# Optimization experiments

Hardware: AMD Instinct MI355X
Metric: run time of the kernel (lower is better)

## Reference

```python
import jax, jax.numpy as jnp
import numpy as np

PAD = 1  # deform_conv2d called with stride=1, padding=1, dilation=1 in forward


def _bilinear_gather(x, py, px):
    """Bilinear sample x [B,C,H,W] at float coords py,px [B,K,Ho,Wo].
    Out-of-bounds corners contribute zero (torchvision deform_conv2d semantics).
    Returns [B,C,K,Ho,Wo]."""
    B, C, H, W = x.shape
    y0 = jnp.floor(py)
    x0 = jnp.floor(px)
    y1, x1 = y0 + 1.0, x0 + 1.0
    wy1 = py - y0
    wy0 = 1.0 - wy1
    wx1 = px - x0
    wx0 = 1.0 - wx1
    x_flat = x.reshape(B, C, H * W)

    def corner(yi, xi, w):
        m = ((yi >= 0) & (yi < H) & (xi >= 0) & (xi < W)).astype(x.dtype)
        yc = jnp.clip(yi, 0, H - 1).astype(jnp.int32)
        xc = jnp.clip(xi, 0, W - 1).astype(jnp.int32)
        lin = (yc * W + xc).reshape(B, -1)  # [B, K*Ho*Wo]
        vals = jax.vmap(lambda xf, idx: jnp.take(xf, idx, axis=1))(x_flat, lin)
        vals = vals.reshape(B, C, *yi.shape[1:])  # [B,C,K,Ho,Wo]
        return vals * (w * m)[:, None]

    return (corner(y0, x0, wy0 * wx0) + corner(y0, x1, wy0 * wx1)
            + corner(y1, x0, wy1 * wx0) + corner(y1, x1, wy1 * wx1))


def reference(x, w_off, b_off, weight):
    B, C, H, W = x.shape
    O, Ci, kh, kw = weight.shape
    K = kh * kw
    # offset conv: Conv2d(C -> 2*k*k, kernel 3, stride 1, pad 1, groups=1)
    offset = jax.lax.conv_general_dilated(
        x, w_off, window_strides=(1, 1), padding=[(PAD, PAD), (PAD, PAD)],
        dimension_numbers=('NCHW', 'OIHW', 'NCHW')) + b_off[None, :, None, None]
    off = offset.reshape(B, K, 2, H, W)  # channel layout: (tap, [dy, dx])

    ky = jnp.repeat(jnp.arange(kh, dtype=x.dtype), kw)  # [K] kernel row index
    kx = jnp.tile(jnp.arange(kw, dtype=x.dtype), kh)    # [K] kernel col index
    ys = jnp.arange(H, dtype=x.dtype)[None, None, :, None]  # [1,1,H,1]
    xs = jnp.arange(W, dtype=x.dtype)[None, None, None, :]  # [1,1,1,W]
    py = ys + (ky - PAD)[None, :, None, None] + off[:, :, 0]  # [B,K,H,W]
    px = xs + (kx - PAD)[None, :, None, None] + off[:, :, 1]

    sampled = _bilinear_gather(x, py, px)  # [B,C,K,H,W]
    out = jnp.einsum('bckhw,ock->bohw', sampled, weight.reshape(O, Ci, K))
    return out


def setup_inputs() -> dict:
    key = jax.random.key(0)
    k1, k2, k3 = jax.random.split(key, 3)
    x = jax.random.normal(k1, (4, 64, 128, 128), dtype=jnp.float32)
    # small offset-conv weights -> modest learned offsets (realistic DCN behavior)
    w_off = jax.random.normal(k2, (18, 64, 3, 3), dtype=jnp.float32) * 0.01
    b_off = jnp.zeros((18,), dtype=jnp.float32)
    weight = jax.random.normal(k3, (64, 64, 3, 3), dtype=jnp.float32)
    return {'x': x, 'w_off': w_off, 'b_off': b_off, 'weight': weight}
```

## Files before the change

### kernel.cpp

```cpp
#include <hip/hip_runtime.h>
#include <math.h>

typedef _Float16 f16;
typedef _Float16 f16x8 __attribute__((ext_vector_type(8)));
typedef float f32x4 __attribute__((ext_vector_type(4)));

namespace {
constexpr int Bn = 4;
constexpr int Cn = 64;
constexpr int On = 64;
constexpr int Hn = 128;
constexpr int Wn = 128;
constexpr int Kn = 9;
constexpr int HWn = Hn * Wn;
constexpr int CKn = Cn * Kn;
constexpr int NPIX = Bn * HWn;
constexpr int SR = 72;
}

__global__ __launch_bounds__(256) void prep_weights(
    const float* __restrict__ w_off, const float* __restrict__ weight,
    f16* __restrict__ wofb, f16* __restrict__ wtb) {
  int t = blockIdx.x * 256 + threadIdx.x;
  if (t < Kn * On * Cn) {
    int c = t & 63, o = (t >> 6) & 63, k = t >> 12;
    wtb[t] = (f16)weight[((o << 6) + c) * 9 + k];
  }
  if (t < Kn * 32 * Cn) {
    int c = t & 63, o = (t >> 6) & 31, k = t >> 11;
    float v = (o < 18) ? w_off[((o << 6) + c) * 9 + k] : 0.f;
    wofb[t] = (f16)v;
  }
}

__global__ __launch_bounds__(256) void transpose_x(
    const float* __restrict__ x, f16* __restrict__ xt) {
  const int l = threadIdx.x & 63;
  const int cw = threadIdx.x >> 6;
  const int pixbase = blockIdx.x * 64;
  const int b = pixbase >> 14;
  const int hw = (pixbase & (HWn - 1)) + l;

  f16x8 v0, v1;
#pragma unroll
  for (int i = 0; i < 8; ++i) {
    v0[i] = (f16)x[((size_t)(b * Cn + cw * 16 + i)) * HWn + hw];
    v1[i] = (f16)x[((size_t)(b * Cn + cw * 16 + 8 + i)) * HWn + hw];
  }
  f16* dst = xt + ((size_t)(b * HWn + hw)) * 64 + cw * 16;
  *(f16x8*)dst = v0;
  *(f16x8*)(dst + 8) = v1;
}

__global__ __launch_bounds__(256) void offset_mfma(
    const f16* __restrict__ xt, const f16* __restrict__ wofb,
    const float* __restrict__ b_off, float* __restrict__ offset) {
  __shared__ __align__(16) f16 Sb[2][64 * SR];
  __shared__ __align__(16) f16 Wb[2][32 * SR];

  const int t = threadIdx.x;
  const int pixbase = blockIdx.x * 64;
  const int b = pixbase >> 14;
  const int y = (pixbase & (HWn - 1)) >> 7;
  const int xx0 = pixbase & (Wn - 1);
  const f16* xb = xt + ((size_t)b * HWn) * 64;

  const int px_s = t >> 2, cq = t & 3;
  const int lane = t & 63, wv = t >> 6;
  const int l15 = lane & 15, q = lane >> 4;
  const int m = wv & 1;
  const int nb = (wv >> 1) * 2;

  auto stage = [&](int k, int buf) {
    const int dy = k / 3 - 1, dx = k % 3 - 1;
    const int ys = y + dy, xs = xx0 + px_s + dx;
    f16* sdst = &Sb[buf][px_s * SR + cq * 16];
    if (ys >= 0 && ys < Hn && xs >= 0 && xs < Wn) {
      const f16* src = xb + (size_t)(ys * Wn + xs) * 64 + cq * 16;
      *(f16x8*)sdst = *(const f16x8*)src;
      *(f16x8*)(sdst + 8) = *(const f16x8*)(src + 8);
    } else {
      f16x8 z = {};
      *(f16x8*)sdst = z;
      *(f16x8*)(sdst + 8) = z;
    }
    const int o = t >> 3, part = t & 7;
    const f16* wsrc = wofb + (((size_t)(k * 32 + o)) << 6) + part * 8;
    *(f16x8*)&Wb[buf][o * SR + part * 8] = *(const f16x8*)wsrc;
  };

  f32x4 acc[2];
#pragma unroll
  for (int t2 = 0; t2 < 2; ++t2) acc[t2] = (f32x4){0.f, 0.f, 0.f, 0.f};

  stage(0, 0);
  __syncthreads();
  for (int k = 0; k < Kn; ++k) {
    const int cur = k & 1;
    if (k + 1 < Kn) stage(k + 1, 1 - cur);
#pragma unroll
    for (int s = 0; s < 2; ++s) {
      f16x8 af = *(const f16x8*)&Wb[cur][(m * 16 + l15) * SR + s * 32 + q * 8];
#pragma unroll
      for (int t2 = 0; t2 < 2; ++t2) {
        f16x8 bf = *(const f16x8*)
            &Sb[cur][((nb + t2) * 16 + l15) * SR + s * 32 + q * 8];
        acc[t2] = __builtin_amdgcn_mfma_f32_16x16x32_f16(af, bf, acc[t2],
                                                         0, 0, 0);
      }
    }
    __syncthreads();
  }

  float* ob = offset + ((size_t)b * HWn + y * Wn + xx0) * 18;
#pragma unroll
  for (int t2 = 0; t2 < 2; ++t2) {
#pragma unroll
    for (int r = 0; r < 4; ++r) {
      int o = m * 16 + q * 4 + r;
      if (o < 18) {
        int pxl = (nb + t2) * 16 + l15;
        ob[(size_t)pxl * 18 + o] = acc[t2][r] + b_off[o];
      }
    }
  }
}

__global__ __launch_bounds__(256, 4) void dcn_main(
    const f16* __restrict__ xt, const float* __restrict__ offset,
    const f16* __restrict__ wtb, float* __restrict__ out) {
  __shared__ __align__(16) f16 Sb[2][64 * SR];
  __shared__ __align__(16) f16 Wb[2][64 * SR];

  const int t = threadIdx.x;
  const int px_s = t >> 2, cq = t & 3;
  const int pxg = blockIdx.x * 64 + px_s;
  const int b = pxg >> 14;
  const int rem = pxg & (HWn - 1);
  const int y = rem >> 7;
  const int xx = rem & (Wn - 1);
  const f16* xb = xt + (((size_t)b) << 14) * 64;

  const int lane = t & 63, wv = t >> 6;
  const int l15 = lane & 15, q = lane >> 4;
  const int obase = wv * 16;

  float2 off9[9];
  {
    const float* ofp = offset + (size_t)pxg * 18;
#pragma unroll
    for (int k = 0; k < Kn; ++k) off9[k] = *(const float2*)(ofp + 2 * k);
  }

  auto stage = [&](int k, int buf) {
    const int dy = k / 3 - 1, dx = k % 3 - 1;
    float py = (float)(y + dy) + off9[k].x;
    float pxf = (float)(xx + dx) + off9[k].y;
    float y0f = floorf(py), x0f = floorf(pxf);
    int y0 = (int)y0f, x0 = (int)x0f;
    int y1 = y0 + 1, x1 = x0 + 1;
    float wy1 = py - y0f, wx1 = pxf - x0f;
    float wy0 = 1.f - wy1, wx0 = 1.f - wx1;
    float my0 = (y0 >= 0 && y0 < Hn) ? 1.f : 0.f;
    float my1 = (y1 >= 0 && y1 < Hn) ? 1.f : 0.f;
    float mx0 = (x0 >= 0 && x0 < Wn) ? 1.f : 0.f;
    float mx1 = (x1 >= 0 && x1 < Wn) ? 1.f : 0.f;
    float w00 = wy0 * wx0 * my0 * mx0;
    float w01 = wy0 * wx1 * my0 * mx1;
    float w10 = wy1 * wx0 * my1 * mx0;
    float w11 = wy1 * wx1 * my1 * mx1;
    int cy0 = min(max(y0, 0), Hn - 1), cy1 = min(max(y1, 0), Hn - 1);
    int cx0 = min(max(x0, 0), Wn - 1), cx1 = min(max(x1, 0), Wn - 1);
    const f16* r00 = xb + (size_t)(cy0 * Wn + cx0) * 64 + cq * 16;
    const f16* r01 = xb + (size_t)(cy0 * Wn + cx1) * 64 + cq * 16;
    const f16* r10 = xb + (size_t)(cy1 * Wn + cx0) * 64 + cq * 16;
    const f16* r11 = xb + (size_t)(cy1 * Wn + cx1) * 64 + cq * 16;
    f16* sdst = &Sb[buf][px_s * SR + cq * 16];
#pragma unroll
    for (int h = 0; h < 2; ++h) {
      f16x8 a = *(const f16x8*)(r00 + h * 8);
      f16x8 bb2 = *(const f16x8*)(r01 + h * 8);
      f16x8 c = *(const f16x8*)(r10 + h * 8);
      f16x8 d = *(const f16x8*)(r11 + h * 8);
      f16x8 v;
#pragma unroll
      for (int i = 0; i < 8; ++i) {
        float s = w00 * (float)a[i] + w01 * (float)bb2[i] +
                  w10 * (float)c[i] + w11 * (float)d[i];
        v[i] = (f16)s;
      }
      *(f16x8*)(sdst + h * 8) = v;
    }
    {
      const int o = t >> 2, part = t & 3;
      const f16* src = wtb + (((size_t)(k * 64 + o)) << 6) + part * 16;
      f16* dst = &Wb[buf][o * SR + part * 16];
      *(f16x8*)dst = *(const f16x8*)src;
      *(f16x8*)(dst + 8) = *(const f16x8*)(src + 8);
    }
  };

  f32x4 acc[4];
#pragma unroll
  for (int pt = 0; pt < 4; ++pt) acc[pt] = (f32x4){0.f, 0.f, 0.f, 0.f};

  stage(0, 0);
  __syncthreads();
  for (int k = 0; k < Kn; ++k) {
    const int cur = k & 1;
    if (k + 1 < Kn) stage(k + 1, 1 - cur);
#pragma unroll
    for (int s = 0; s < 2; ++s) {
      f16x8 af = *(const f16x8*)&Wb[cur][(obase + l15) * SR + s * 32 + q * 8];
#pragma unroll
      for (int pt = 0; pt < 4; ++pt) {
        f16x8 bf =
            *(const f16x8*)&Sb[cur][(pt * 16 + l15) * SR + s * 32 + q * 8];
        acc[pt] = __builtin_amdgcn_mfma_f32_16x16x32_f16(af, bf, acc[pt],
                                                         0, 0, 0);
      }
    }
    __syncthreads();
  }

  const int hw0 = (blockIdx.x * 64) & (HWn - 1);
  const int bb = (blockIdx.x * 64) >> 14;
  float* ob = out + (size_t)bb * On * HWn + hw0;
#pragma unroll
  for (int pt = 0; pt < 4; ++pt) {
#pragma unroll
    for (int r = 0; r < 4; ++r) {
      int o = obase + q * 4 + r;
      ob[(size_t)o * HWn + pt * 16 + l15] = acc[pt][r];
    }
  }
}

extern "C" void kernel_launch(void* const* d_in, const int* in_sizes, int n_in,
                              void* d_out, int out_size, void* d_ws, size_t ws_size,
                              hipStream_t stream) {
  const float* x = (const float*)d_in[0];
  const float* w_off = (const float*)d_in[1];
  const float* b_off = (const float*)d_in[2];
  const float* weight = (const float*)d_in[3];
  float* out = (float*)d_out;

  f16* xt = (f16*)d_ws;
  float* offset = (float*)(xt + (size_t)NPIX * Cn);
  f16* wtb = (f16*)(offset + (size_t)NPIX * 18);
  f16* wofb = wtb + Kn * On * Cn;

  prep_weights<<<dim3(144), dim3(256), 0, stream>>>(w_off, weight, wofb, wtb);
  transpose_x<<<dim3(NPIX / 64), dim3(256), 0, stream>>>(x, xt);
  offset_mfma<<<dim3(NPIX / 64), dim3(256), 0, stream>>>(xt, wofb, b_off,
                                                         offset);
  dcn_main<<<dim3(NPIX / 64), dim3(256), 0, stream>>>(xt, offset, wtb, out);
}
```

Measured before the change: 113.0 us.

## Fuse offset conv into deformable main kernel and merge weight prep into transpose

Merges the weight-prep kernel into the x transpose kernel and fuses the offset-conv MFMA kernel with the deformable gather/GEMM kernel. Offsets now pass through shared memory instead of a global buffer, which removes one global round trip and two launches. The shared-memory staging of weights is replaced by direct per-lane register loads from global memory, prefetched one tap ahead. This cuts LDS use and barriers but adds global weight reads to every wave. It also relies on the weight-prep blocks finishing before the fused kernel starts, which stream ordering guarantees.

```diff
diff --git a/kernel.cpp b/kernel.cpp
--- a/kernel.cpp
+++ b/kernel.cpp
@@ -13,15 +13,15 @@
 constexpr int Wn = 128;
 constexpr int Kn = 9;
 constexpr int HWn = Hn * Wn;
-constexpr int CKn = Cn * Kn;
 constexpr int NPIX = Bn * HWn;
 constexpr int SR = 72;
 }
 
-__global__ __launch_bounds__(256) void prep_weights(
-    const float* __restrict__ w_off, const float* __restrict__ weight,
+__global__ __launch_bounds__(256) void transpose_prep(
+    const float* __restrict__ x, const float* __restrict__ w_off,
+    const float* __restrict__ weight, f16* __restrict__ xt,
     f16* __restrict__ wofb, f16* __restrict__ wtb) {
-  int t = blockIdx.x * 256 + threadIdx.x;
+  const int t = blockIdx.x * 256 + threadIdx.x;
   if (t < Kn * On * Cn) {
     int c = t & 63, o = (t >> 6) & 63, k = t >> 12;
     wtb[t] = (f16)weight[((o << 6) + c) * 9 + k];
@@ -31,10 +31,7 @@
     float v = (o < 18) ? w_off[((o << 6) + c) * 9 + k] : 0.f;
     wofb[t] = (f16)v;
   }
-}
-
-__global__ __launch_bounds__(256) void transpose_x(
-    const float* __restrict__ x, f16* __restrict__ xt) {
+
   const int l = threadIdx.x & 63;
   const int cw = threadIdx.x >> 6;
   const int pixbase = blockIdx.x * 64;
@@ -52,26 +49,28 @@
   *(f16x8*)(dst + 8) = v1;
 }
 
-__global__ __launch_bounds__(256) void offset_mfma(
+__global__ __launch_bounds__(256, 4) void dcn_fused(
     const f16* __restrict__ xt, const f16* __restrict__ wofb,
-    const float* __restrict__ b_off, float* __restrict__ offset) {
+    const float* __restrict__ b_off, const f16* __restrict__ wtb,
+    float* __restrict__ out) {
   __shared__ __align__(16) f16 Sb[2][64 * SR];
-  __shared__ __align__(16) f16 Wb[2][32 * SR];
+  __shared__ __align__(16) float offL[64 * 18];
 
   const int t = threadIdx.x;
   const int pixbase = blockIdx.x * 64;
   const int b = pixbase >> 14;
   const int y = (pixbase & (HWn - 1)) >> 7;
   const int xx0 = pixbase & (Wn - 1);
-  const f16* xb = xt + ((size_t)b * HWn) * 64;
+  const f16* xb = xt + (((size_t)b) << 14) * 64;
 
   const int px_s = t >> 2, cq = t & 3;
   const int lane = t & 63, wv = t >> 6;
   const int l15 = lane & 15, q = lane >> 4;
+
   const int m = wv & 1;
   const int nb = (wv >> 1) * 2;
 
-  auto stage = [&](int k, int buf) {
+  auto stage1 = [&](int k, int buf) {
     const int dy = k / 3 - 1, dx = k % 3 - 1;
     const int ys = y + dy, xs = xx0 + px_s + dx;
     f16* sdst = &Sb[buf][px_s * SR + cq * 16];
@@ -84,35 +83,39 @@
       *(f16x8*)sdst = z;
       *(f16x8*)(sdst + 8) = z;
     }
-    const int o = t >> 3, part = t & 7;
-    const f16* wsrc = wofb + (((size_t)(k * 32 + o)) << 6) + part * 8;
-    *(f16x8*)&Wb[buf][o * SR + part * 8] = *(const f16x8*)wsrc;
   };
 
-  f32x4 acc[2];
-#pragma unroll
-  for (int t2 = 0; t2 < 2; ++t2) acc[t2] = (f32x4){0.f, 0.f, 0.f, 0.f};
-
-  stage(0, 0);
+  f32x4 acc2[2] = {};
+  f16x8 af[2], afn[2];
+#pragma unroll
+  for (int s = 0; s < 2; ++s)
+    af[s] = *(const f16x8*)&wofb[(size_t)(m * 16 + l15) * 64 + s * 32 + q * 8];
+  stage1(0, 0);
   __syncthreads();
   for (int k = 0; k < Kn; ++k) {
     const int cur = k & 1;
-    if (k + 1 < Kn) stage(k + 1, 1 - cur);
+    if (k + 1 < Kn) {
+      stage1(k + 1, 1 - cur);
+#pragma unroll
+      for (int s = 0; s < 2; ++s)
+        afn[s] = *(const f16x8*)
+            &wofb[(size_t)((k + 1) * 32 + m * 16 + l15) * 64 + s * 32 + q * 8];
+    }
 #pragma unroll
     for (int s = 0; s < 2; ++s) {
-      f16x8 af = *(const f16x8*)&Wb[cur][(m * 16 + l15) * SR + s * 32 + q * 8];
 #pragma unroll
       for (int t2 = 0; t2 < 2; ++t2) {
         f16x8 bf = *(const f16x8*)
             &Sb[cur][((nb + t2) * 16 + l15) * SR + s * 32 + q * 8];
-        acc[t2] = __builtin_amdgcn_mfma_f32_16x16x32_f16(af, bf, acc[t2],
-                                                         0, 0, 0);
+        acc2[t2] = __builtin_amdgcn_mfma_f32_16x16x32_f16(af[s], bf, acc2[t2],
+                                                          0, 0, 0);
       }
     }
     __syncthreads();
-  }
-
-  float* ob = offset + ((size_t)b * HWn + y * Wn + xx0) * 18;
+    af[0] = afn[0];
+    af[1] = afn[1];
+  }
+
 #pragma unroll
   for (int t2 = 0; t2 < 2; ++t2) {
 #pragma unroll
@@ -120,39 +123,23 @@
       int o = m * 16 + q * 4 + r;
       if (o < 18) {
         int pxl = (nb + t2) * 16 + l15;
-        ob[(size_t)pxl * 18 + o] = acc[t2][r] + b_off[o];
-      }
-    }
-  }
-}
-
-__global__ __launch_bounds__(256, 4) void dcn_main(
-    const f16* __restrict__ xt, const float* __restrict__ offset,
-    const f16* __restrict__ wtb, float* __restrict__ out) {
-  __shared__ __align__(16) f16 Sb[2][64 * SR];
-  __shared__ __align__(16) f16 Wb[2][64 * SR];
-
-  const int t = threadIdx.x;
-  const int px_s = t >> 2, cq = t & 3;
-  const int pxg = blockIdx.x * 64 + px_s;
-  const int b = pxg >> 14;
-  const int rem = pxg & (HWn - 1);
-  const int y = rem >> 7;
-  const int xx = rem & (Wn - 1);
-  const f16* xb = xt + (((size_t)b) << 14) * 64;
-
-  const int lane = t & 63, wv = t >> 6;
-  const int l15 = lane & 15, q = lane >> 4;
-  const int obase = wv * 16;
+        offL[pxl * 18 + o] = acc2[t2][r] + b_off[o];
+      }
+    }
+  }
+  __syncthreads();
 
   float2 off9[9];
   {
-    const float* ofp = offset + (size_t)pxg * 18;
-#pragma unroll
-    for (int k = 0; k < Kn; ++k) off9[k] = *(const float2*)(ofp + 2 * k);
-  }
-
-  auto stage = [&](int k, int buf) {
+    const float* op = &offL[px_s * 18];
+#pragma unroll
+    for (int k = 0; k < Kn; ++k) off9[k] = *(const float2*)(op + 2 * k);
+  }
+
+  const int xx = xx0 + px_s;
+  const int obase = wv * 16;
+
+  auto stage2 = [&](int k, int buf) {
     const int dy = k / 3 - 1, dx = k % 3 - 1;
     float py = (float)(y + dy) + off9[k].x;
     float pxf = (float)(xx + dx) + off9[k].y;
@@ -191,41 +178,40 @@
       }
       *(f16x8*)(sdst + h * 8) = v;
     }
-    {
-      const int o = t >> 2, part = t & 3;
-      const f16* src = wtb + (((size_t)(k * 64 + o)) << 6) + part * 16;
-      f16* dst = &Wb[buf][o * SR + part * 16];
-      *(f16x8*)dst = *(const f16x8*)src;
-      *(f16x8*)(dst + 8) = *(const f16x8*)(src + 8);
-    }
   };
 
-  f32x4 acc[4];
-#pragma unroll
-  for (int pt = 0; pt < 4; ++pt) acc[pt] = (f32x4){0.f, 0.f, 0.f, 0.f};
-
-  stage(0, 0);
+  f32x4 acc[4] = {};
+  f16x8 wf[2], wfn[2];
+#pragma unroll
+  for (int s = 0; s < 2; ++s)
+    wf[s] = *(const f16x8*)&wtb[(size_t)(obase + l15) * 64 + s * 32 + q * 8];
+  stage2(0, 0);
   __syncthreads();
   for (int k = 0; k < Kn; ++k) {
     const int cur = k & 1;
-    if (k + 1 < Kn) stage(k + 1, 1 - cur);
+    if (k + 1 < Kn) {
+      stage2(k + 1, 1 - cur);
+#pragma unroll
+      for (int s = 0; s < 2; ++s)
+        wfn[s] = *(const f16x8*)
+            &wtb[(size_t)((k + 1) * 64 + obase + l15) * 64 + s * 32 + q * 8];
+    }
 #pragma unroll
     for (int s = 0; s < 2; ++s) {
-      f16x8 af = *(const f16x8*)&Wb[cur][(obase + l15) * SR + s * 32 + q * 8];
 #pragma unroll
       for (int pt = 0; pt < 4; ++pt) {
         f16x8 bf =
             *(const f16x8*)&Sb[cur][(pt * 16 + l15) * SR + s * 32 + q * 8];
-        acc[pt] = __builtin_amdgcn_mfma_f32_16x16x32_f16(af, bf, acc[pt],
+        acc[pt] = __builtin_amdgcn_mfma_f32_16x16x32_f16(wf[s], bf, acc[pt],
                                                          0, 0, 0);
       }
     }
     __syncthreads();
-  }
-
-  const int hw0 = (blockIdx.x * 64) & (HWn - 1);
-  const int bb = (blockIdx.x * 64) >> 14;
-  float* ob = out + (size_t)bb * On * HWn + hw0;
+    wf[0] = wfn[0];
+    wf[1] = wfn[1];
+  }
+
+  float* ob = out + (size_t)b * On * HWn + (pixbase & (HWn - 1));
 #pragma unroll
   for (int pt = 0; pt < 4; ++pt) {
 #pragma unroll
@@ -237,8 +223,8 @@
 }
 
 extern "C" void kernel_launch(void* const* d_in, const int* in_sizes, int n_in,
-                              void* d_out, int out_size, void* d_ws, size_t ws_size,
-                              hipStream_t stream) {
+                              void* d_out, int out_size, void* d_ws,
+                              size_t ws_size, hipStream_t stream) {
   const float* x = (const float*)d_in[0];
   const float* w_off = (const float*)d_in[1];
   const float* b_off = (const float*)d_in[2];
@@ -246,13 +232,11 @@
   float* out = (float*)d_out;
 
   f16* xt = (f16*)d_ws;
-  float* offset = (float*)(xt + (size_t)NPIX * Cn);
-  f16* wtb = (f16*)(offset + (size_t)NPIX * 18);
+  f16* wtb = xt + (size_t)NPIX * Cn;
   f16* wofb = wtb + Kn * On * Cn;
 
-  prep_weights<<<dim3(144), dim3(256), 0, stream>>>(w_off, weight, wofb, wtb);
-  transpose_x<<<dim3(NPIX / 64), dim3(256), 0, stream>>>(x, xt);
-  offset_mfma<<<dim3(NPIX / 64), dim3(256), 0, stream>>>(xt, wofb, b_off,
-                                                         offset);
-  dcn_main<<<dim3(NPIX / 64), dim3(256), 0, stream>>>(xt, offset, wtb, out);
-}
+  transpose_prep<<<dim3(NPIX / 64), dim3(256), 0, stream>>>(x, w_off, weight,
+                                                            xt, wofb, wtb);
+  dcn_fused<<<dim3(NPIX / 64), dim3(256), 0, stream>>>(xt, wofb, b_off, wtb,
+                                                       out);
+}
```

Result: faster. 110.1 us (-2.6%).
